# Optimization experiments

Measured on AMD Instinct MI355X. Metric: run time of the kernel, lower is better.

The kernel has to match this reference:

```python
import jax, jax.numpy as jnp
import numpy as np

TOP_K = 2
NUM_EXPERTS = 64


def setup_inputs() -> dict:
    key = jax.random.key(0)
    k1, k2, k3 = jax.random.split(key, 3)
    T, D, E = 16384, 2048, NUM_EXPERTS
    x = jax.random.normal(k1, (T, D), dtype=jnp.float32)
    # gate projection weight (the _forward of the concrete router)
    w_gate = jax.random.normal(k2, (D, E), dtype=jnp.float32) * (1.0 / np.sqrt(D))
    # gate.perturbation(scores.shape, NORMAL): additive Gaussian noise, materialized for determinism
    noise = jax.random.normal(k3, (T, E), dtype=jnp.float32)
    return {"x": x, "w_gate": w_gate, "noise": noise}


def reference(x, w_gate, noise):
    T, E = x.shape[0], w_gate.shape[1]
    # _forward: expert scores [T, E]
    scores = x @ w_gate
    # gate.compute on perturbed scores: softmax -> top-k -> renormalized gates
    probs = jax.nn.softmax(scores + noise, axis=-1)
    topk_vals, topk_idx = jax.lax.top_k(probs, TOP_K)          # [T, k]
    gates = topk_vals / jnp.sum(topk_vals, axis=-1, keepdims=True)
    # combine tensor [T, E]: gate weight scattered to the chosen experts
    rows = jnp.arange(T)[:, None]                               # [T, 1]
    combine = jnp.zeros((T, E), dtype=gates.dtype).at[rows, topk_idx].add(gates)
    # _track_expert_activations: scatter_add of ones per selected expert column
    expert_activation = jnp.zeros((E,), dtype=jnp.float32).at[topk_idx.ravel()].add(1.0)
    return combine, topk_idx, gates, expert_activation
```

## Files before the change

kernel.cpp:

```cpp
#include <hip/hip_runtime.h>
#include <math.h>

#define T_TOKENS 16384
#define DIM      2048
#define NEXP     64
#define TOPK     2

#define NKC   4
#define NEG   4
#define EPG   (NEXP / NEG)
#define KC    (DIM / NKC)
#define PSTR  68

#define OFF_COMBINE 0
#define OFF_IDX     (T_TOKENS * NEXP)
#define OFF_GATES   (OFF_IDX + T_TOKENS * TOPK)
#define OFF_ACT     (OFF_GATES + T_TOKENS * TOPK)

__global__ void zero_act_kernel(float* __restrict__ out) {
    int i = threadIdx.x;
    if (i < NEXP) out[OFF_ACT + i] = 0.0f;
}

struct Acc { float4 a0, a1, a2, a3; };

__device__ __forceinline__ void fma16(Acc& A, float xs, const float* __restrict__ wr) {
    const float4 w0 = *reinterpret_cast<const float4*>(wr + 0);
    const float4 w1 = *reinterpret_cast<const float4*>(wr + 4);
    const float4 w2 = *reinterpret_cast<const float4*>(wr + 8);
    const float4 w3 = *reinterpret_cast<const float4*>(wr + 12);
    A.a0.x = fmaf(xs, w0.x, A.a0.x); A.a0.y = fmaf(xs, w0.y, A.a0.y);
    A.a0.z = fmaf(xs, w0.z, A.a0.z); A.a0.w = fmaf(xs, w0.w, A.a0.w);
    A.a1.x = fmaf(xs, w1.x, A.a1.x); A.a1.y = fmaf(xs, w1.y, A.a1.y);
    A.a1.z = fmaf(xs, w1.z, A.a1.z); A.a1.w = fmaf(xs, w1.w, A.a1.w);
    A.a2.x = fmaf(xs, w2.x, A.a2.x); A.a2.y = fmaf(xs, w2.y, A.a2.y);
    A.a2.z = fmaf(xs, w2.z, A.a2.z); A.a2.w = fmaf(xs, w2.w, A.a2.w);
    A.a3.x = fmaf(xs, w3.x, A.a3.x); A.a3.y = fmaf(xs, w3.y, A.a3.y);
    A.a3.z = fmaf(xs, w3.z, A.a3.z); A.a3.w = fmaf(xs, w3.w, A.a3.w);
}

__device__ __forceinline__ void fma16x4(Acc& A, float4 xv, const float* __restrict__ wr) {
    fma16(A, xv.x, wr);
    fma16(A, xv.y, wr + NEXP);
    fma16(A, xv.z, wr + 2 * NEXP);
    fma16(A, xv.w, wr + 3 * NEXP);
}

__global__ __launch_bounds__(1024, 4)
void router_kernel(const float* __restrict__ x,
                   const float* __restrict__ w,
                   const float* __restrict__ noise,
                   float* __restrict__ out) {
    __shared__ float part[NKC][64][PSTR];
    __shared__ float nsh[64][PSTR];
    __shared__ float g1s[64], g2s[64];
    __shared__ int   i1s[64], i2s[64];
    __shared__ float bins[NEXP];

    const int tid  = threadIdx.x;
    const int lane = tid & 63;
    const int wv   = __builtin_amdgcn_readfirstlane(tid >> 6);
    const int eg   = wv & (NEG - 1);
    const int kc   = wv >> 2;
    const int row  = blockIdx.x * 64 + lane;
    const int k0   = kc * KC;

    if (tid < NEXP) bins[tid] = 0.0f;

    {
        const int r = tid >> 4, c = (tid & 15) * 4;
        const float4 nv = *reinterpret_cast<const float4*>(
            noise + (size_t)(blockIdx.x * 64 + r) * NEXP + c);
        *reinterpret_cast<float4*>(&nsh[r][c]) = nv;
    }

    Acc A;
    A.a0 = make_float4(0.f, 0.f, 0.f, 0.f);
    A.a1 = A.a0; A.a2 = A.a0; A.a3 = A.a0;

    const float* __restrict__ xp = x + (size_t)row * DIM + k0;
    const float* __restrict__ wp = w + (size_t)k0 * NEXP + eg * EPG;

    float4 X0 = *reinterpret_cast<const float4*>(xp + 0);
    float4 X1 = *reinterpret_cast<const float4*>(xp + 4);
    float4 X2 = *reinterpret_cast<const float4*>(xp + 8);
    float4 X3 = *reinterpret_cast<const float4*>(xp + 12);
    float4 Y0 = *reinterpret_cast<const float4*>(xp + 16);
    float4 Y1 = *reinterpret_cast<const float4*>(xp + 20);
    float4 Y2 = *reinterpret_cast<const float4*>(xp + 24);
    float4 Y3 = *reinterpret_cast<const float4*>(xp + 28);

    #pragma unroll 1
    for (int kk = 0; kk < KC; kk += 16) {
        const int kpre = (kk + 32 < KC) ? (kk + 32) : 0;
        const float4 Z0 = *reinterpret_cast<const float4*>(xp + kpre + 0);
        const float4 Z1 = *reinterpret_cast<const float4*>(xp + kpre + 4);
        const float4 Z2 = *reinterpret_cast<const float4*>(xp + kpre + 8);
        const float4 Z3 = *reinterpret_cast<const float4*>(xp + kpre + 12);

        const float* __restrict__ wr = wp + (size_t)kk * NEXP;
        fma16x4(A, X0, wr);
        fma16x4(A, X1, wr + 4 * NEXP);
        fma16x4(A, X2, wr + 8 * NEXP);
        fma16x4(A, X3, wr + 12 * NEXP);

        X0 = Y0; X1 = Y1; X2 = Y2; X3 = Y3;
        Y0 = Z0; Y1 = Z1; Y2 = Z2; Y3 = Z3;
    }

    {
        float* pr = &part[kc][lane][eg * EPG];
        *reinterpret_cast<float4*>(pr + 0)  = A.a0;
        *reinterpret_cast<float4*>(pr + 4)  = A.a1;
        *reinterpret_cast<float4*>(pr + 8)  = A.a2;
        *reinterpret_cast<float4*>(pr + 12) = A.a3;
    }
    __syncthreads();

    if (wv == 0) {
        const int r = lane;
        float m1 = -1e30f, m2 = -1e30f;
        int i1 = 0, i2 = 0;
        #pragma unroll
        for (int j = 0; j < NEXP; j += 4) {
            float4 s        = *reinterpret_cast<const float4*>(&part[0][r][j]);
            const float4 p1 = *reinterpret_cast<const float4*>(&part[1][r][j]);
            const float4 p2 = *reinterpret_cast<const float4*>(&part[2][r][j]);
            const float4 p3 = *reinterpret_cast<const float4*>(&part[3][r][j]);
            const float4 nv = *reinterpret_cast<const float4*>(&nsh[r][j]);
            s.x += p1.x + p2.x + p3.x + nv.x;
            s.y += p1.y + p2.y + p3.y + nv.y;
            s.z += p1.z + p2.z + p3.z + nv.z;
            s.w += p1.w + p2.w + p3.w + nv.w;
            if (s.x > m1) { m2 = m1; i2 = i1; m1 = s.x; i1 = j + 0; } else if (s.x > m2) { m2 = s.x; i2 = j + 0; }
            if (s.y > m1) { m2 = m1; i2 = i1; m1 = s.y; i1 = j + 1; } else if (s.y > m2) { m2 = s.y; i2 = j + 1; }
            if (s.z > m1) { m2 = m1; i2 = i1; m1 = s.z; i1 = j + 2; } else if (s.z > m2) { m2 = s.z; i2 = j + 2; }
            if (s.w > m1) { m2 = m1; i2 = i1; m1 = s.w; i1 = j + 3; } else if (s.w > m2) { m2 = s.w; i2 = j + 3; }
        }

        const float t  = expf(m2 - m1);
        const float g1 = 1.0f / (1.0f + t);
        const float g2 = 1.0f - g1;

        out[OFF_IDX + row * 2 + 0]   = (float)i1;
        out[OFF_IDX + row * 2 + 1]   = (float)i2;
        out[OFF_GATES + row * 2 + 0] = g1;
        out[OFF_GATES + row * 2 + 1] = g2;

        g1s[r] = g1; g2s[r] = g2; i1s[r] = i1; i2s[r] = i2;
        atomicAdd(&bins[i1], 1.0f);
        atomicAdd(&bins[i2], 1.0f);
    }
    __syncthreads();

    {
        const int r = tid >> 4, c = (tid & 15) * 4;
        const int   a  = i1s[r], b = i2s[r];
        const float ga = g1s[r], gb = g2s[r];
        float4 v;
        v.x = (c + 0 == a) ? ga : (c + 0 == b) ? gb : 0.0f;
        v.y = (c + 1 == a) ? ga : (c + 1 == b) ? gb : 0.0f;
        v.z = (c + 2 == a) ? ga : (c + 2 == b) ? gb : 0.0f;
        v.w = (c + 3 == a) ? ga : (c + 3 == b) ? gb : 0.0f;
        *reinterpret_cast<float4*>(
            out + OFF_COMBINE + (size_t)(blockIdx.x * 64 + r) * NEXP + c) = v;
    }

    if (tid < NEXP) {
        const float v = bins[tid];
        if (v != 0.0f) atomicAdd(out + OFF_ACT + tid, v);
    }
}

extern "C" void kernel_launch(void* const* d_in, const int* in_sizes, int n_in,
                              void* d_out, int out_size, void* d_ws, size_t ws_size,
                              hipStream_t stream) {
    const float* x     = (const float*)d_in[0];
    const float* wg    = (const float*)d_in[1];
    const float* noise = (const float*)d_in[2];
    float* out = (float*)d_out;

    zero_act_kernel<<<1, 64, 0, stream>>>(out);
    router_kernel<<<T_TOKENS / 64, 1024, 0, stream>>>(x, wg, noise, out);
}
```

Measured before the change: 244.5 us.

## Split K across two blocks per tile and add a separate top-k finish kernel

The fused router kernel is replaced by a GEMM kernel that splits the 2048-long reduction over two blocks per 64-row tile, giving 512 blocks instead of 256. Each block writes its partial scores either into the combine output region or into a workspace buffer. A second kernel sums the two partials with the noise and does the top-2 selection, gates, combine and activation counts. This aims to fill more CUs during the memory-bound GEMM, at the cost of an extra round trip of partial scores through global memory and one more launch.

```diff
diff --git a/kernel.cpp b/kernel.cpp
--- a/kernel.cpp
+++ b/kernel.cpp
@@ -6,21 +6,17 @@
 #define NEXP     64
 #define TOPK     2
 
+#define KB    1024
 #define NKC   4
 #define NEG   4
 #define EPG   (NEXP / NEG)
-#define KC    (DIM / NKC)
-#define PSTR  68
+#define KC    (KB / NKC)
+#define XS    68
 
 #define OFF_COMBINE 0
 #define OFF_IDX     (T_TOKENS * NEXP)
 #define OFF_GATES   (OFF_IDX + T_TOKENS * TOPK)
 #define OFF_ACT     (OFF_GATES + T_TOKENS * TOPK)
-
-__global__ void zero_act_kernel(float* __restrict__ out) {
-    int i = threadIdx.x;
-    if (i < NEXP) out[OFF_ACT + i] = 0.0f;
-}
 
 struct Acc { float4 a0, a1, a2, a3; };
 
@@ -46,33 +42,24 @@
     fma16(A, xv.w, wr + 3 * NEXP);
 }
 
-__global__ __launch_bounds__(1024, 4)
-void router_kernel(const float* __restrict__ x,
-                   const float* __restrict__ w,
-                   const float* __restrict__ noise,
-                   float* __restrict__ out) {
-    __shared__ float part[NKC][64][PSTR];
-    __shared__ float nsh[64][PSTR];
-    __shared__ float g1s[64], g2s[64];
-    __shared__ int   i1s[64], i2s[64];
-    __shared__ float bins[NEXP];
+__global__ __launch_bounds__(1024, 8)
+void gemm_kernel(const float* __restrict__ x,
+                 const float* __restrict__ w,
+                 float* __restrict__ out,
+                 float* __restrict__ p1) {
+    __shared__ float part[NKC][64][XS];
 
     const int tid  = threadIdx.x;
     const int lane = tid & 63;
     const int wv   = __builtin_amdgcn_readfirstlane(tid >> 6);
     const int eg   = wv & (NEG - 1);
-    const int kc   = wv >> 2;
-    const int row  = blockIdx.x * 64 + lane;
-    const int k0   = kc * KC;
+    const int sub  = wv >> 2;
+    const int tile = blockIdx.x >> 1;
+    const int kc   = blockIdx.x & 1;
+    const int k0   = kc * KB + sub * KC;
+    const int row  = tile * 64 + lane;
 
-    if (tid < NEXP) bins[tid] = 0.0f;
-
-    {
-        const int r = tid >> 4, c = (tid & 15) * 4;
-        const float4 nv = *reinterpret_cast<const float4*>(
-            noise + (size_t)(blockIdx.x * 64 + r) * NEXP + c);
-        *reinterpret_cast<float4*>(&nsh[r][c]) = nv;
-    }
+    if (blockIdx.x == 0 && tid < NEXP) out[OFF_ACT + tid] = 0.0f;
 
     Acc A;
     A.a0 = make_float4(0.f, 0.f, 0.f, 0.f);
@@ -109,61 +96,86 @@
     }
 
     {
-        float* pr = &part[kc][lane][eg * EPG];
+        float* pr = &part[sub][lane][eg * EPG];
         *reinterpret_cast<float4*>(pr + 0)  = A.a0;
         *reinterpret_cast<float4*>(pr + 4)  = A.a1;
         *reinterpret_cast<float4*>(pr + 8)  = A.a2;
         *reinterpret_cast<float4*>(pr + 12) = A.a3;
     }
     __syncthreads();
+    {
+        const int sr = tid >> 4, sc = (tid & 15) * 4;
+        float4 pa       = *reinterpret_cast<const float4*>(&part[0][sr][sc]);
+        const float4 p1v = *reinterpret_cast<const float4*>(&part[1][sr][sc]);
+        const float4 p2v = *reinterpret_cast<const float4*>(&part[2][sr][sc]);
+        const float4 p3v = *reinterpret_cast<const float4*>(&part[3][sr][sc]);
+        pa.x += p1v.x + p2v.x + p3v.x;
+        pa.y += p1v.y + p2v.y + p3v.y;
+        pa.z += p1v.z + p2v.z + p3v.z;
+        pa.w += p1v.w + p2v.w + p3v.w;
+        float* __restrict__ pd = kc ? p1 : (out + OFF_COMBINE);
+        *reinterpret_cast<float4*>(pd + (size_t)(tile * 64 + sr) * NEXP + sc) = pa;
+    }
+}
 
-    if (wv == 0) {
-        const int r = lane;
+__global__ __launch_bounds__(1024)
+void finish_kernel(const float* __restrict__ p1,
+                   const float* __restrict__ noise,
+                   float* __restrict__ out) {
+    __shared__ float lg[64][XS];
+    __shared__ float g1s[64], g2s[64];
+    __shared__ int   i1s[64], i2s[64];
+    __shared__ float bins[NEXP];
+
+    const int tid = threadIdx.x;
+    const int r = tid >> 4, c = (tid & 15) * 4;
+    const size_t rowbase = (size_t)(blockIdx.x * 64 + r) * NEXP + c;
+
+    float4 a       = *reinterpret_cast<const float4*>(out + OFF_COMBINE + rowbase);
+    const float4 b = *reinterpret_cast<const float4*>(p1 + rowbase);
+    const float4 n = *reinterpret_cast<const float4*>(noise + rowbase);
+    a.x += b.x + n.x; a.y += b.y + n.y; a.z += b.z + n.z; a.w += b.w + n.w;
+    *reinterpret_cast<float4*>(&lg[r][c]) = a;
+    if (tid < NEXP) bins[tid] = 0.0f;
+    __syncthreads();
+
+    if (tid < 64) {
+        const int rr = tid;
         float m1 = -1e30f, m2 = -1e30f;
         int i1 = 0, i2 = 0;
         #pragma unroll
         for (int j = 0; j < NEXP; j += 4) {
-            float4 s        = *reinterpret_cast<const float4*>(&part[0][r][j]);
-            const float4 p1 = *reinterpret_cast<const float4*>(&part[1][r][j]);
-            const float4 p2 = *reinterpret_cast<const float4*>(&part[2][r][j]);
-            const float4 p3 = *reinterpret_cast<const float4*>(&part[3][r][j]);
-            const float4 nv = *reinterpret_cast<const float4*>(&nsh[r][j]);
-            s.x += p1.x + p2.x + p3.x + nv.x;
-            s.y += p1.y + p2.y + p3.y + nv.y;
-            s.z += p1.z + p2.z + p3.z + nv.z;
-            s.w += p1.w + p2.w + p3.w + nv.w;
+            const float4 s = *reinterpret_cast<const float4*>(&lg[rr][j]);
             if (s.x > m1) { m2 = m1; i2 = i1; m1 = s.x; i1 = j + 0; } else if (s.x > m2) { m2 = s.x; i2 = j + 0; }
             if (s.y > m1) { m2 = m1; i2 = i1; m1 = s.y; i1 = j + 1; } else if (s.y > m2) { m2 = s.y; i2 = j + 1; }
             if (s.z > m1) { m2 = m1; i2 = i1; m1 = s.z; i1 = j + 2; } else if (s.z > m2) { m2 = s.z; i2 = j + 2; }
             if (s.w > m1) { m2 = m1; i2 = i1; m1 = s.w; i1 = j + 3; } else if (s.w > m2) { m2 = s.w; i2 = j + 3; }
         }
-
         const float t  = expf(m2 - m1);
         const float g1 = 1.0f / (1.0f + t);
         const float g2 = 1.0f - g1;
 
+        const int row = blockIdx.x * 64 + rr;
         out[OFF_IDX + row * 2 + 0]   = (float)i1;
         out[OFF_IDX + row * 2 + 1]   = (float)i2;
         out[OFF_GATES + row * 2 + 0] = g1;
         out[OFF_GATES + row * 2 + 1] = g2;
 
-        g1s[r] = g1; g2s[r] = g2; i1s[r] = i1; i2s[r] = i2;
+        g1s[rr] = g1; g2s[rr] = g2; i1s[rr] = i1; i2s[rr] = i2;
         atomicAdd(&bins[i1], 1.0f);
         atomicAdd(&bins[i2], 1.0f);
     }
     __syncthreads();
 
     {
-        const int r = tid >> 4, c = (tid & 15) * 4;
-        const int   a  = i1s[r], b = i2s[r];
+        const int   ia = i1s[r], ib = i2s[r];
         const float ga = g1s[r], gb = g2s[r];
         float4 v;
-        v.x = (c + 0 == a) ? ga : (c + 0 == b) ? gb : 0.0f;
-        v.y = (c + 1 == a) ? ga : (c + 1 == b) ? gb : 0.0f;
-        v.z = (c + 2 == a) ? ga : (c + 2 == b) ? gb : 0.0f;
-        v.w = (c + 3 == a) ? ga : (c + 3 == b) ? gb : 0.0f;
-        *reinterpret_cast<float4*>(
-            out + OFF_COMBINE + (size_t)(blockIdx.x * 64 + r) * NEXP + c) = v;
+        v.x = (c + 0 == ia) ? ga : (c + 0 == ib) ? gb : 0.0f;
+        v.y = (c + 1 == ia) ? ga : (c + 1 == ib) ? gb : 0.0f;
+        v.z = (c + 2 == ia) ? ga : (c + 2 == ib) ? gb : 0.0f;
+        v.w = (c + 3 == ia) ? ga : (c + 3 == ib) ? gb : 0.0f;
+        *reinterpret_cast<float4*>(out + OFF_COMBINE + rowbase) = v;
     }
 
     if (tid < NEXP) {
@@ -179,7 +191,8 @@
     const float* wg    = (const float*)d_in[1];
     const float* noise = (const float*)d_in[2];
     float* out = (float*)d_out;
+    float* p1  = (float*)d_ws;
 
-    zero_act_kernel<<<1, 64, 0, stream>>>(out);
-    router_kernel<<<T_TOKENS / 64, 1024, 0, stream>>>(x, wg, noise, out);
+    gemm_kernel<<<512, 1024, 0, stream>>>(x, wg, out, p1);
+    finish_kernel<<<T_TOKENS / 64, 1024, 0, stream>>>(p1, noise, out);
 }
```

New measurement: 254.6 us. +4.1%, slower.
